# Kernel tuning notes

Measured on AMD Instinct MI355X. Metric: run time of the kernel, lower is better.

The kernel has to match this reference:

```python
import jax, jax.numpy as jnp
import numpy as np

N, E, D, L, NE, FF, G, V, H = 4096, 131072, 256, 4, 2, 512, 128, 100, 8
DK = D // H


def setup_inputs() -> dict:
    key = jax.random.key(0)
    ks = iter(jax.random.split(key, 64))
    def W(shape, scale=0.05):
        return jax.random.normal(next(ks), shape, dtype=jnp.float32) * scale
    inp = {}
    inp['z'] = jax.random.randint(next(ks), (N,), 0, V)
    inp['pos'] = jax.random.normal(next(ks), (N, 3), dtype=jnp.float32)
    inp['batch'] = jnp.sort(jax.random.randint(next(ks), (N,), 0, G))
    inp['edge_index'] = jax.random.randint(next(ks), (2, E), 0, N)
    inp['emb'] = W((V, D))
    # E_GCL stacks (EGNN layer: edge MLP, attention gate, node MLP)
    inp['egcl_edge_w1'] = W((L, 2 * D + 1, D)); inp['egcl_edge_b1'] = jnp.zeros((L, D), jnp.float32)
    inp['egcl_edge_w2'] = W((L, D, D));         inp['egcl_edge_b2'] = jnp.zeros((L, D), jnp.float32)
    inp['egcl_node_w1'] = W((L, 2 * D, D));     inp['egcl_node_b1'] = jnp.zeros((L, D), jnp.float32)
    inp['egcl_node_w2'] = W((L, D, D));         inp['egcl_node_b2'] = jnp.zeros((L, D), jnp.float32)
    inp['egcl_att_w'] = W((L, D, 1));           inp['egcl_att_b'] = jnp.zeros((L, 1), jnp.float32)
    # Transformer encoder stacks (post-norm)
    inp['enc_wq'] = W((NE, D, D)); inp['enc_bq'] = jnp.zeros((NE, D), jnp.float32)
    inp['enc_wk'] = W((NE, D, D)); inp['enc_bk'] = jnp.zeros((NE, D), jnp.float32)
    inp['enc_wv'] = W((NE, D, D)); inp['enc_bv'] = jnp.zeros((NE, D), jnp.float32)
    inp['enc_wo'] = W((NE, D, D)); inp['enc_bo'] = jnp.zeros((NE, D), jnp.float32)
    inp['enc_ln1_g'] = jnp.ones((NE, D), jnp.float32); inp['enc_ln1_b'] = jnp.zeros((NE, D), jnp.float32)
    inp['enc_ffn_w1'] = W((NE, D, FF)); inp['enc_ffn_b1'] = jnp.zeros((NE, FF), jnp.float32)
    inp['enc_ffn_w2'] = W((NE, FF, D)); inp['enc_ffn_b2'] = jnp.zeros((NE, D), jnp.float32)
    inp['enc_ln2_g'] = jnp.ones((NE, D), jnp.float32); inp['enc_ln2_b'] = jnp.zeros((NE, D), jnp.float32)
    # energy_fc head
    inp['fc_w1'] = W((D, D)); inp['fc_b1'] = jnp.zeros((D,), jnp.float32)
    inp['fc_w2'] = W((D, 1)); inp['fc_b2'] = jnp.zeros((1,), jnp.float32)
    return inp


def _layer_norm(x, g, b, eps=1e-5):
    mu = jnp.mean(x, axis=-1, keepdims=True)
    var = jnp.mean((x - mu) ** 2, axis=-1, keepdims=True)
    return (x - mu) * jax.lax.rsqrt(var + eps) * g + b


def reference(z, pos, batch, edge_index, emb,
              egcl_edge_w1, egcl_edge_b1, egcl_edge_w2, egcl_edge_b2,
              egcl_node_w1, egcl_node_b1, egcl_node_w2, egcl_node_b2,
              egcl_att_w, egcl_att_b,
              enc_wq, enc_bq, enc_wk, enc_bk, enc_wv, enc_bv, enc_wo, enc_bo,
              enc_ln1_g, enc_ln1_b, enc_ffn_w1, enc_ffn_b1, enc_ffn_w2, enc_ffn_b2,
              enc_ln2_g, enc_ln2_b, fc_w1, fc_b1, fc_w2, fc_b2):
    h = emb[z]                                   # [N, D]
    row, col = edge_index[0], edge_index[1]
    diff = pos[row] - pos[col]                   # static_coord: coords never updated
    radial = jnp.sum(diff * diff, axis=-1, keepdims=True)  # [E, 1]
    for i in range(L):
        m_in = jnp.concatenate([h[row], h[col], radial], axis=-1)     # [E, 2D+1]
        m = jax.nn.silu(m_in @ egcl_edge_w1[i] + egcl_edge_b1[i])
        m = jax.nn.silu(m @ egcl_edge_w2[i] + egcl_edge_b2[i])        # [E, D]
        m = m * jax.nn.sigmoid(m @ egcl_att_w[i] + egcl_att_b[i])     # attention gate
        agg = jax.ops.segment_sum(m, row, num_segments=N)             # [N, D]
        n_in = jnp.concatenate([h, agg], axis=-1)
        upd = jax.nn.silu(n_in @ egcl_node_w1[i] + egcl_node_b1[i]) @ egcl_node_w2[i] + egcl_node_b2[i]
        h = h + upd                                                   # residual
    scale = 1.0 / jnp.sqrt(jnp.asarray(DK, h.dtype))
    for i in range(NE):
        q = (h @ enc_wq[i] + enc_bq[i]).reshape(N, H, DK)
        k = (h @ enc_wk[i] + enc_bk[i]).reshape(N, H, DK)
        v = (h @ enc_wv[i] + enc_bv[i]).reshape(N, H, DK)
        scores = jnp.einsum('nhd,mhd->hnm', q, k) * scale
        a = jax.nn.softmax(scores, axis=-1)
        attn = jnp.einsum('hnm,mhd->nhd', a, v).reshape(N, D) @ enc_wo[i] + enc_bo[i]
        h = _layer_norm(h + attn, enc_ln1_g[i], enc_ln1_b[i])
        f = jax.nn.silu(h @ enc_ffn_w1[i] + enc_ffn_b1[i]) @ enc_ffn_w2[i] + enc_ffn_b2[i]
        h = _layer_norm(h + f, enc_ln2_g[i], enc_ln2_b[i])
    g = jax.ops.segment_sum(h, batch, num_segments=G)                 # scatter-add readout
    out = jax.nn.silu(g @ fc_w1 + fc_b1) @ fc_w2 + fc_b2              # [G, 1]
    return out
```

## Files before the change

### kernel.cpp

```cpp
#include <hip/hip_runtime.h>
#include <math.h>

#define N_NODES 4096
#define N_EDGES 131072
#define DIM     256
#define NL      4
#define NENC    2
#define FFD     512
#define NG      128
#define NHEAD   8
#define DKH     32
#define TE2     32

typedef __attribute__((ext_vector_type(8))) short bf16x8;
typedef __attribute__((ext_vector_type(4))) float f32x4;

__device__ __forceinline__ float siluf(float x) { return x / (1.f + __expf(-x)); }
__device__ __forceinline__ float sigmf_(float x) { return 1.f / (1.f + __expf(-x)); }
__device__ __forceinline__ unsigned short f2b(float f) {
    union { float f; unsigned u; } x; x.f = f;
    unsigned r = x.u + 0x7fffu + ((x.u >> 16) & 1u);
    return (unsigned short)(r >> 16);
}
__device__ __forceinline__ float b2f(unsigned short h) {
    union { unsigned u; float f; } x; x.u = (unsigned)h << 16; return x.f;
}

__global__ __launch_bounds__(256) void k_embed(const int* __restrict__ z,
                                               const float* __restrict__ emb,
                                               float* __restrict__ h) {
    int i = blockIdx.x * 256 + threadIdx.x;
    int n = i >> 8, d = i & 255;
    h[i] = emb[z[n] * DIM + d];
}

__global__ __launch_bounds__(256) void k_radial(const float* __restrict__ pos,
                                                const int* __restrict__ ei,
                                                float* __restrict__ radial) {
    int e = blockIdx.x * 256 + threadIdx.x;
    if (e >= N_EDGES) return;
    int r = ei[e], c = ei[N_EDGES + e];
    float dx = pos[r*3+0] - pos[c*3+0];
    float dy = pos[r*3+1] - pos[c*3+1];
    float dz = pos[r*3+2] - pos[c*3+2];
    radial[e] = dx*dx + dy*dy + dz*dz;
}

__global__ __launch_bounds__(256) void k_hist(const int* __restrict__ ei, int* __restrict__ cnt) {
    int e = blockIdx.x * 256 + threadIdx.x;
    if (e < N_EDGES) atomicAdd(&cnt[ei[e]], 1);
}

__global__ __launch_bounds__(256) void k_scan(const int* __restrict__ cnt, int* __restrict__ pos) {
    __shared__ int s_w[4];
    int t = threadIdx.x, lane = t & 63, wv = t >> 6;
    int loc[16]; int s = 0;
    #pragma unroll
    for (int i = 0; i < 16; ++i) { loc[i] = s; s += cnt[t * 16 + i]; }
    int inc = s;
    #pragma unroll
    for (int off = 1; off < 64; off <<= 1) {
        int v = __shfl_up(inc, off, 64);
        if (lane >= off) inc += v;
    }
    if (lane == 63) s_w[wv] = inc;
    __syncthreads();
    int wbase = 0;
    for (int j = 0; j < wv; ++j) wbase += s_w[j];
    int base = wbase + inc - s;
    #pragma unroll
    for (int i = 0; i < 16; ++i) pos[t * 16 + i] = base + loc[i];
}

__global__ __launch_bounds__(256) void k_scatter(const int* __restrict__ ei,
                                                 const float* __restrict__ radial,
                                                 int* __restrict__ pos,
                                                 int* __restrict__ rows_s,
                                                 int* __restrict__ cols_s,
                                                 float* __restrict__ rad_s) {
    int e = blockIdx.x * 256 + threadIdx.x;
    if (e >= N_EDGES) return;
    int r = ei[e];
    int p = atomicAdd(&pos[r], 1);
    rows_s[p] = r;
    cols_s[p] = ei[N_EDGES + e];
    rad_s[p] = radial[e];
}

__global__ __launch_bounds__(256) void k_conv_w2(const float* __restrict__ ew2,
                                                 unsigned short* __restrict__ W2F) {
    int tid = blockIdx.x * 256 + threadIdx.x;
    int layer = tid >> 13;
    int r = tid & 8191;
    int ks = r >> 10, ntg = (r >> 6) & 15, lane = r & 63;
    const float* W = ew2 + (size_t)layer * 65536;
    unsigned short tmp[8];
    #pragma unroll
    for (int j = 0; j < 8; ++j) {
        int k = ks*32 + 4*(lane>>4) + (j&3) + 16*(j>>2);
        int n = ntg*16 + (lane&15);
        tmp[j] = f2b(W[k*256 + n]);
    }
    *(bf16x8*)&W2F[(size_t)layer*65536 + (size_t)r*8] = *(const bf16x8*)&tmp[0];
}

__global__ __launch_bounds__(256) void k_pack_all(
    const float* __restrict__ ew1, const float* __restrict__ nw1, const float* __restrict__ nw2,
    const float* __restrict__ wq, const float* __restrict__ wk, const float* __restrict__ wv,
    const float* __restrict__ wo, const float* __restrict__ fw1, const float* __restrict__ fw2,
    unsigned short* __restrict__ dst)
{
    int f = blockIdx.x * 256 + threadIdx.x;
    int rem, panel, NTG, mode;
    if (f < 65536)       { rem = f;          panel = rem / 16384; rem &= 16383; NTG = 32; mode = 0; }
    else if (f < 131072) { rem = f - 65536;  panel = rem / 16384; rem &= 16383; NTG = 16; mode = 1; }
    else if (f < 163840) { rem = f - 131072; panel = rem / 8192;  rem &= 8191;  NTG = 16; mode = 2; }
    else if (f < 212992) { rem = f - 163840; panel = rem / 24576; rem %= 24576; NTG = 48; mode = 3; }
    else if (f < 229376) { rem = f - 212992; panel = rem / 8192;  rem &= 8191;  NTG = 16; mode = 4; }
    else if (f < 262144) { rem = f - 229376; panel = rem / 16384; rem &= 16383; NTG = 32; mode = 5; }
    else                 { rem = f - 262144; panel = rem / 16384; rem &= 16383; NTG = 16; mode = 6; }
    int ks   = rem / (NTG * 64);
    int ntg  = (rem >> 6) % NTG;
    int lane = rem & 63;
    unsigned short tmp[8];
    #pragma unroll
    for (int j = 0; j < 8; ++j) {
        int k = ks*32 + 4*(lane>>4) + (j&3) + 16*(j>>2);
        int n = ntg*16 + (lane&15);
        float val;
        switch (mode) {
            case 0: val = ew1[(size_t)panel*131328 + (n < 256 ? k*256 + n : (256 + k)*256 + (n - 256))]; break;
            case 1: val = nw1[(size_t)panel*131072 + k*256 + n]; break;
            case 2: val = nw2[(size_t)panel*65536 + k*256 + n]; break;
            case 3: { const float* b = (n < 256) ? wq : ((n < 512) ? wk : wv);
                      val = b[(size_t)panel*65536 + k*256 + (n & 255)]; } break;
            case 4: val = wo[(size_t)panel*65536 + k*256 + n]; break;
            case 5: val = fw1[(size_t)panel*131072 + k*512 + n]; break;
            default: val = fw2[(size_t)panel*131072 + k*256 + n]; break;
        }
        tmp[j] = f2b(val);
    }
    *(bf16x8*)&dst[(size_t)f * 8] = *(const bf16x8*)&tmp[0];
}

template<int NCHUNK, int NC, int NSPLIT, int ACT, int RESID, int OUTMODE>
__global__ __launch_bounds__(256) void k_gemm(
    const float* __restrict__ A0, const float* __restrict__ A1, int lda,
    const unsigned short* __restrict__ Wp,
    const float* __restrict__ b0, const float* __restrict__ b1, const float* __restrict__ b2,
    const float* __restrict__ resid, float* __restrict__ C,
    unsigned short* __restrict__ kpk, unsigned short* __restrict__ vpk)
{
    constexpr int NT  = NC / (64 * NSPLIT);
    constexpr int NTG = NC / 16;
    __shared__ __align__(16) char s_hi[16 * 512];
    __shared__ __align__(16) char s_lo[16 * 512];
    const int t = threadIdx.x, l = t & 63, w = t >> 6;
    const int g = l >> 4, r = l & 15;
    const int mtile  = blockIdx.x % 256;
    const int nchunk = blockIdx.x / 256;
    const int r0 = mtile * 16;

    f32x4 acc[NT];
    #pragma unroll
    for (int nt = 0; nt < NT; ++nt) acc[nt] = (f32x4){0.f, 0.f, 0.f, 0.f};

    const bf16x8* Wf = (const bf16x8*)Wp;
    for (int c = 0; c < NCHUNK; ++c) {
        const float* Ac = (c == 0) ? A0 : A1;
        __syncthreads();
        const int c4 = l * 4;
        #pragma unroll
        for (int it = 0; it < 4; ++it) {
            int row = it * 4 + w;
            float4 v = *(const float4*)&Ac[(size_t)(r0 + row) * lda + c4];
            float vv[4] = {v.x, v.y, v.z, v.w};
            ushort4 h4, l4;
            unsigned short hh;
            hh = f2b(vv[0]); h4.x = hh; l4.x = f2b(vv[0] - b2f(hh));
            hh = f2b(vv[1]); h4.y = hh; l4.y = f2b(vv[1] - b2f(hh));
            hh = f2b(vv[2]); h4.z = hh; l4.z = f2b(vv[2] - b2f(hh));
            hh = f2b(vv[3]); h4.w = hh; l4.w = f2b(vv[3] - b2f(hh));
            int boff = (c4 * 2) ^ (row << 3);
            *(ushort4*)&s_hi[row * 512 + boff] = h4;
            *(ushort4*)&s_lo[row * 512 + boff] = l4;
        }
        __syncthreads();
        #pragma unroll
        for (int ks = 0; ks < 8; ++ks) {
            const int ksg = c * 8 + ks;
            const int x0 = (ks * 64 + 8 * g) ^ (r << 3);
            union { uint2 u[2]; bf16x8 v; } ah, al;
            ah.u[0] = *(const uint2*)&s_hi[r * 512 + x0];
            ah.u[1] = *(const uint2*)&s_hi[r * 512 + (x0 ^ 32)];
            al.u[0] = *(const uint2*)&s_lo[r * 512 + x0];
            al.u[1] = *(const uint2*)&s_lo[r * 512 + (x0 ^ 32)];
            #pragma unroll
            for (int nt = 0; nt < NT; ++nt) {
                int fb = (nchunk * 4 + w) * NT + nt;
                bf16x8 bf_ = Wf[(size_t)(ksg * NTG + fb) * 64 + l];
                acc[nt] = __builtin_amdgcn_mfma_f32_16x16x32_bf16(ah.v, bf_, acc[nt], 0, 0, 0);
                acc[nt] = __builtin_amdgcn_mfma_f32_16x16x32_bf16(al.v, bf_, acc[nt], 0, 0, 0);
            }
        }
    }
    #pragma unroll
    for (int nt = 0; nt < NT; ++nt) {
        int n = ((nchunk * 4 + w) * NT + nt) * 16 + r;
        float bias = 0.f;
        if (b0) {
            const float* bp = (n < 256) ? b0 : ((n < 512) ? b1 : b2);
            bias = bp[n & 255];
        }
        #pragma unroll
        for (int reg = 0; reg < 4; ++reg) {
            int row = r0 + g * 4 + reg;
            float v = acc[nt][reg] + bias;
            if (ACT == 1) v = siluf(v);
            if (RESID) v += resid[(size_t)row * 256 + n];
            if (OUTMODE == 0) {
                C[(size_t)row * NC + n] = v;
            } else {
                if (n < 256) {
                    C[(size_t)row * 256 + n] = v;
                } else if (n < 512) {
                    int hd = (n - 256) >> 5, dm = (n - 256) & 31;
                    int dp = (dm & 3) | (((dm >> 4) & 1) << 2) | (((dm >> 2) & 3) << 3);
                    unsigned short hb = f2b(v);
                    size_t base = ((size_t)hd * N_NODES + row) * 64;
                    kpk[base + dp]      = hb;
                    kpk[base + 32 + dp] = f2b(v - b2f(hb));
                } else {
                    int hd = (n - 512) >> 5, dm = (n - 512) & 31;
                    int s = row & 31;
                    int sp = (s & 3) | (((s >> 4) & 1) << 2) | (((s >> 2) & 3) << 3);
                    int keyp = (row & ~31) | sp;
                    vpk[((size_t)hd * 32 + dm) * N_NODES + keyp] = f2b(v);
                }
            }
        }
    }
}

__global__ __launch_bounds__(256) void k_edge_mfma(
    const float* __restrict__ P12,
    const int* __restrict__ rows_s, const int* __restrict__ cols_s,
    const float* __restrict__ rad_s,
    const float* __restrict__ w1r, const float* __restrict__ b1,
    const unsigned short* __restrict__ W2F, const float* __restrict__ b2,
    const float* __restrict__ aw, const float* __restrict__ ab,
    float* __restrict__ agg)
{
    __shared__ __align__(16) char s_a[TE2 * 512];
    __shared__ int   s_row[TE2], s_cn[TE2];
    __shared__ float s_rad[TE2], s_gp[4][TE2], s_gate[TE2];
    const int t = threadIdx.x, l = t & 63, w = t >> 6;
    const int e0 = blockIdx.x * TE2;

    if (t < TE2) {
        s_row[t] = rows_s[e0 + t];
        s_cn[t]  = cols_s[e0 + t];
        s_rad[t] = rad_s[e0 + t];
    }
    __syncthreads();

    const int c4 = l * 4;
    const float4 wr = *(const float4*)&w1r[c4];
    const float4 bb = *(const float4*)&b1[c4];
    #pragma unroll
    for (int it = 0; it < 8; ++it) {
        int e = it * 4 + w;
        float4 pa = *(const float4*)&P12[(size_t)s_row[e] * 512 + c4];
        float4 pb = *(const float4*)&P12[(size_t)s_cn[e] * 512 + 256 + c4];
        float rad = s_rad[e];
        ushort4 pk;
        pk.x = f2b(siluf(pa.x + pb.x + rad * wr.x + bb.x));
        pk.y = f2b(siluf(pa.y + pb.y + rad * wr.y + bb.y));
        pk.z = f2b(siluf(pa.z + pb.z + rad * wr.z + bb.z));
        pk.w = f2b(siluf(pa.w + pb.w + rad * wr.w + bb.w));
        *(ushort4*)&s_a[e * 512 + ((c4 * 2) ^ ((e & 15) << 3))] = pk;
    }
    __syncthreads();

    const int g = l >> 4, r = l & 15;
    f32x4 acc[2][4];
    #pragma unroll
    for (int mt = 0; mt < 2; ++mt)
        #pragma unroll
        for (int nt = 0; nt < 4; ++nt)
            acc[mt][nt] = (f32x4){0.f, 0.f, 0.f, 0.f};

    const bf16x8* Wf = (const bf16x8*)W2F;
    for (int ks = 0; ks < 8; ++ks) {
        bf16x8 af[2], bfr[4];
        #pragma unroll
        for (int mt = 0; mt < 2; ++mt) {
            int rowa = mt * 16 + r;
            int x0 = (ks * 64 + 8 * g) ^ (r << 3);
            uint2 lo = *(const uint2*)&s_a[rowa * 512 + x0];
            uint2 hi = *(const uint2*)&s_a[rowa * 512 + (x0 ^ 32)];
            union { uint2 u[2]; bf16x8 v; } ua;
            ua.u[0] = lo; ua.u[1] = hi;
            af[mt] = ua.v;
        }
        #pragma unroll
        for (int nt = 0; nt < 4; ++nt)
            bfr[nt] = Wf[(ks * 16 + w * 4 + nt) * 64 + l];
        #pragma unroll
        for (int mt = 0; mt < 2; ++mt)
            #pragma unroll
            for (int nt = 0; nt < 4; ++nt)
                acc[mt][nt] = __builtin_amdgcn_mfma_f32_16x16x32_bf16(af[mt], bfr[nt], acc[mt][nt], 0, 0, 0);
    }

    float b2v[4], awv[4];
    #pragma unroll
    for (int nt = 0; nt < 4; ++nt) {
        int col = w * 64 + nt * 16 + r;
        b2v[nt] = b2[col];
        awv[nt] = aw[col];
    }
    float pg[2][4];
    #pragma unroll
    for (int mt = 0; mt < 2; ++mt)
        #pragma unroll
        for (int reg = 0; reg < 4; ++reg) {
            float s = 0.f;
            #pragma unroll
            for (int nt = 0; nt < 4; ++nt) {
                float v = siluf(acc[mt][nt][reg] + b2v[nt]);
                acc[mt][nt][reg] = v;
                s += v * awv[nt];
            }
            pg[mt][reg] = s;
        }
    #pragma unroll
    for (int off = 1; off < 16; off <<= 1)
        #pragma unroll
        for (int mt = 0; mt < 2; ++mt)
            #pragma unroll
            for (int reg = 0; reg < 4; ++reg)
                pg[mt][reg] += __shfl_xor(pg[mt][reg], off, 64);
    if (r == 0) {
        #pragma unroll
        for (int mt = 0; mt < 2; ++mt)
            #pragma unroll
            for (int reg = 0; reg < 4; ++reg)
                s_gp[w][mt * 16 + g * 4 + reg] = pg[mt][reg];
    }
    __syncthreads();
    if (t < TE2)
        s_gate[t] = sigmf_(s_gp[0][t] + s_gp[1][t] + s_gp[2][t] + s_gp[3][t] + ab[0]);
    __syncthreads();

    unsigned short* s_out = (unsigned short*)s_a;
    #pragma unroll
    for (int mt = 0; mt < 2; ++mt)
        #pragma unroll
        for (int reg = 0; reg < 4; ++reg) {
            int el = mt * 16 + g * 4 + reg;
            float gt = s_gate[el];
            #pragma unroll
            for (int nt = 0; nt < 4; ++nt)
                s_out[el * 256 + w * 64 + nt * 16 + r] = f2b(acc[mt][nt][reg] * gt);
        }
    __syncthreads();
    float cur = 0.f;
    for (int e = 0; e < TE2; ++e) {
        cur += b2f(s_out[e * 256 + t]);
        bool flush = (e == TE2 - 1) || (s_row[e + 1] != s_row[e]);
        if (flush) {
            atomicAdd(&agg[(size_t)s_row[e] * DIM + t], cur);
            cur = 0.f;
        }
    }
}

template<int ACT>
__global__ __launch_bounds__(256) void k_mlp_small(
    const float* __restrict__ A1, const float* __restrict__ W,
    const float* __restrict__ bias, float* __restrict__ C)
{
    __shared__ float s_a[16][260];
    const int t  = threadIdx.x;
    const int r0 = blockIdx.x * 16;
    for (int r = 0; r < 16; ++r)
        s_a[r][t] = A1[(size_t)(r0 + r) * DIM + t];
    __syncthreads();
    const int er0 = (t >> 6) * 4;
    const int c0 = (t & 63) * 4;
    float acc[4][4];
    #pragma unroll
    for (int e = 0; e < 4; ++e)
        #pragma unroll
        for (int c = 0; c < 4; ++c) acc[e][c] = 0.f;
    #pragma unroll 2
    for (int k = 0; k < DIM; k += 4) {
        float4 w0 = *(const float4*)&W[(size_t)(k+0)*DIM + c0];
        float4 w1 = *(const float4*)&W[(size_t)(k+1)*DIM + c0];
        float4 w2 = *(const float4*)&W[(size_t)(k+2)*DIM + c0];
        float4 w3 = *(const float4*)&W[(size_t)(k+3)*DIM + c0];
        #pragma unroll
        for (int e = 0; e < 4; ++e) {
            float4 x = *(const float4*)&s_a[er0+e][k];
            acc[e][0] += x.x*w0.x + x.y*w1.x + x.z*w2.x + x.w*w3.x;
            acc[e][1] += x.x*w0.y + x.y*w1.y + x.z*w2.y + x.w*w3.y;
            acc[e][2] += x.x*w0.z + x.y*w1.z + x.z*w2.z + x.w*w3.z;
            acc[e][3] += x.x*w0.w + x.y*w1.w + x.z*w2.w + x.w*w3.w;
        }
    }
    float4 bb = *(const float4*)&bias[c0];
    #pragma unroll
    for (int e = 0; e < 4; ++e) {
        float v0 = acc[e][0] + bb.x, v1 = acc[e][1] + bb.y;
        float v2 = acc[e][2] + bb.z, v3 = acc[e][3] + bb.w;
        if (ACT == 1) { v0 = siluf(v0); v1 = siluf(v1); v2 = siluf(v2); v3 = siluf(v3); }
        float4 o; o.x = v0; o.y = v1; o.z = v2; o.w = v3;
        *(float4*)&C[(size_t)(r0 + er0 + e) * DIM + c0] = o;
    }
}

__global__ __launch_bounds__(256) void k_ln(const float* __restrict__ x,
                                            const float* __restrict__ g,
                                            const float* __restrict__ b,
                                            float* __restrict__ out) {
    int t = threadIdx.x, lane = t & 63, w = t >> 6;
    int row = blockIdx.x * 4 + w;
    float4 v = *(const float4*)&x[(size_t)row * DIM + lane * 4];
    float s = v.x + v.y + v.z + v.w;
    #pragma unroll
    for (int off = 32; off; off >>= 1) s += __shfl_xor(s, off, 64);
    float mu = s * (1.f / 256.f);
    float dx = v.x - mu, dy = v.y - mu, dz = v.z - mu, dw = v.w - mu;
    float q = dx*dx + dy*dy + dz*dz + dw*dw;
    #pragma unroll
    for (int off = 32; off; off >>= 1) q += __shfl_xor(q, off, 64);
    float rs = rsqrtf(q * (1.f / 256.f) + 1e-5f);
    float4 gg = *(const float4*)&g[lane * 4];
    float4 bb = *(const float4*)&b[lane * 4];
    float4 o;
    o.x = dx * rs * gg.x + bb.x;
    o.y = dy * rs * gg.y + bb.y;
    o.z = dz * rs * gg.z + bb.z;
    o.w = dw * rs * gg.w + bb.w;
    *(float4*)&out[(size_t)row * DIM + lane * 4] = o;
}

__global__ __launch_bounds__(256) void k_attn_mfma(
    const float* __restrict__ q,
    const unsigned short* __restrict__ kpk,
    const unsigned short* __restrict__ vpk,
    float* __restrict__ o)
{
    __shared__ __align__(16) char s_k[2][8192];
    __shared__ __align__(16) char s_v[2][4096];
    const int t = threadIdx.x, lane = t & 63, w = t >> 6;
    const int g = lane >> 4, r = lane & 15;
    const int head = blockIdx.y;
    const int q0 = blockIdx.x * 64;
    const float scale = 0.17677669529663687f;

    bf16x8 qh, ql;
    {
        const float* qp = &q[(size_t)(q0 + w*16 + r) * DIM + head*DKH + 4*g];
        float4 f0 = *(const float4*)qp;
        float4 f1 = *(const float4*)(qp + 16);
        float vv[8] = {f0.x, f0.y, f0.z, f0.w, f1.x, f1.y, f1.z, f1.w};
        union { unsigned short s[8]; bf16x8 v; } uh, ul;
        #pragma unroll
        for (int j = 0; j < 8; ++j) {
            float sv = vv[j] * scale;
            unsigned short hb = f2b(sv);
            uh.s[j] = hb;
            ul.s[j] = f2b(sv - b2f(hb));
        }
        qh = uh.v; ql = ul.v;
    }

    const char* kbase = (const char*)(kpk + (size_t)head * N_NODES * 64);
    const unsigned short* vbase = vpk + (size_t)head * 32 * N_NODES;
    const int vrow = t >> 3, vch = t & 7;

    uint4 kr0, kr1, vr0;
    {
        const char* kt = kbase;
        kr0 = *(const uint4*)(kt + t * 16);
        kr1 = *(const uint4*)(kt + 4096 + t * 16);
        vr0 = *(const uint4*)(vbase + (size_t)vrow * N_NODES + vch * 8);
        int key0 = t >> 3, sl0 = t & 7;
        *(uint4*)&s_k[0][key0 * 128 + ((sl0 ^ (key0 & 7)) << 4)] = kr0;
        int c1 = t + 256, key1 = c1 >> 3, sl1 = c1 & 7;
        *(uint4*)&s_k[0][key1 * 128 + ((sl1 ^ (key1 & 7)) << 4)] = kr1;
        *(uint4*)&s_v[0][vrow * 128 + ((vch ^ (vrow & 7)) << 4)] = vr0;
    }
    __syncthreads();

    float m = -1e30f, l = 0.f;
    f32x4 ot0 = (f32x4){0.f,0.f,0.f,0.f}, ot1 = (f32x4){0.f,0.f,0.f,0.f};

    for (int tile = 0; tile < 64; ++tile) {
        const int cur = tile & 1;
        if (tile < 63) {
            const char* kt = kbase + (size_t)(tile + 1) * 8192;
            kr0 = *(const uint4*)(kt + t * 16);
            kr1 = *(const uint4*)(kt + 4096 + t * 16);
            vr0 = *(const uint4*)(vbase + (size_t)vrow * N_NODES + (tile + 1) * 64 + vch * 8);
        }
        bf16x8 kh[4], kl[4];
        #pragma unroll
        for (int kb = 0; kb < 4; ++kb) {
            int key = kb * 16 + r;
            kh[kb] = *(const bf16x8*)&s_k[cur][key * 128 + ((g ^ (r & 7)) << 4)];
            kl[kb] = *(const bf16x8*)&s_k[cur][key * 128 + (((4 + g) ^ (r & 7)) << 4)];
        }
        f32x4 sc[4];
        #pragma unroll
        for (int kb = 0; kb < 4; ++kb) {
            f32x4 a = (f32x4){0.f,0.f,0.f,0.f};
            a = __builtin_amdgcn_mfma_f32_16x16x32_bf16(kh[kb], qh, a, 0, 0, 0);
            a = __builtin_amdgcn_mfma_f32_16x16x32_bf16(kh[kb], ql, a, 0, 0, 0);
            a = __builtin_amdgcn_mfma_f32_16x16x32_bf16(kl[kb], qh, a, 0, 0, 0);
            sc[kb] = a;
        }
        float tm = -1e30f;
        #pragma unroll
        for (int kb = 0; kb < 4; ++kb)
            #pragma unroll
            for (int e = 0; e < 4; ++e) tm = fmaxf(tm, sc[kb][e]);
        tm = fmaxf(tm, __shfl_xor(tm, 16, 64));
        tm = fmaxf(tm, __shfl_xor(tm, 32, 64));
        float nm = fmaxf(m, tm);
        float scf = __expf(m - nm);
        m = nm;
        float p[16]; float ls = 0.f;
        #pragma unroll
        for (int kb = 0; kb < 4; ++kb)
            #pragma unroll
            for (int e = 0; e < 4; ++e) {
                float pe = __expf(sc[kb][e] - nm);
                p[kb*4+e] = pe; ls += pe;
            }
        ls += __shfl_xor(ls, 16, 64);
        ls += __shfl_xor(ls, 32, 64);
        l = l * scf + ls;
        ot0[0] *= scf; ot0[1] *= scf; ot0[2] *= scf; ot0[3] *= scf;
        ot1[0] *= scf; ot1[1] *= scf; ot1[2] *= scf; ot1[3] *= scf;
        union { unsigned short s[8]; bf16x8 v; } pk0, pk1;
        #pragma unroll
        for (int j = 0; j < 8; ++j) {
            pk0.s[j] = f2b(p[(j >> 2) * 4 + (j & 3)]);
            pk1.s[j] = f2b(p[(2 + (j >> 2)) * 4 + (j & 3)]);
        }
        bf16x8 vf00 = *(const bf16x8*)&s_v[cur][(0*16 + r) * 128 + (((0*4 + g) ^ (r & 7)) << 4)];
        bf16x8 vf01 = *(const bf16x8*)&s_v[cur][(0*16 + r) * 128 + (((1*4 + g) ^ (r & 7)) << 4)];
        bf16x8 vf10 = *(const bf16x8*)&s_v[cur][(1*16 + r) * 128 + (((0*4 + g) ^ (r & 7)) << 4)];
        bf16x8 vf11 = *(const bf16x8*)&s_v[cur][(1*16 + r) * 128 + (((1*4 + g) ^ (r & 7)) << 4)];
        ot0 = __builtin_amdgcn_mfma_f32_16x16x32_bf16(vf00, pk0.v, ot0, 0, 0, 0);
        ot0 = __builtin_amdgcn_mfma_f32_16x16x32_bf16(vf01, pk1.v, ot0, 0, 0, 0);
        ot1 = __builtin_amdgcn_mfma_f32_16x16x32_bf16(vf10, pk0.v, ot1, 0, 0, 0);
        ot1 = __builtin_amdgcn_mfma_f32_16x16x32_bf16(vf11, pk1.v, ot1, 0, 0, 0);

        __syncthreads();
        if (tile < 63) {
            int key0 = t >> 3, sl0 = t & 7;
            *(uint4*)&s_k[cur ^ 1][key0 * 128 + ((sl0 ^ (key0 & 7)) << 4)] = kr0;
            int c1 = t + 256, key1 = c1 >> 3, sl1 = c1 & 7;
            *(uint4*)&s_k[cur ^ 1][key1 * 128 + ((sl1 ^ (key1 & 7)) << 4)] = kr1;
            *(uint4*)&s_v[cur ^ 1][vrow * 128 + ((vch ^ (vrow & 7)) << 4)] = vr0;
        }
        __syncthreads();
    }

    float inv = 1.f / l;
    float* op = &o[(size_t)(q0 + w*16 + r) * DIM + head*DKH];
    *(float4*)(op + 4*g)      = make_float4(ot0[0]*inv, ot0[1]*inv, ot0[2]*inv, ot0[3]*inv);
    *(float4*)(op + 16 + 4*g) = make_float4(ot1[0]*inv, ot1[1]*inv, ot1[2]*inv, ot1[3]*inv);
}

__global__ __launch_bounds__(256) void k_segsum(const float* __restrict__ h,
                                                const int* __restrict__ batch,
                                                float* __restrict__ gbuf) {
    int i = blockIdx.x * 256 + threadIdx.x;
    int n = i >> 8, d = i & 255;
    atomicAdd(&gbuf[batch[n] * DIM + d], h[i]);
}

__global__ __launch_bounds__(256) void k_head2(const float* __restrict__ gmid,
                                               const float* __restrict__ w2,
                                               const float* __restrict__ b2,
                                               float* __restrict__ out) {
    int t = threadIdx.x, lane = t & 63, w = t >> 6;
    int g = blockIdx.x * 4 + w;
    float4 x  = *(const float4*)&gmid[g * DIM + lane * 4];
    float4 ww = *(const float4*)&w2[lane * 4];
    float s = x.x * ww.x + x.y * ww.y + x.z * ww.z + x.w * ww.w;
    #pragma unroll
    for (int off = 32; off; off >>= 1) s += __shfl_xor(s, off, 64);
    if (lane == 0) out[g] = s + b2[0];
}

extern "C" void kernel_launch(void* const* d_in, const int* in_sizes, int n_in,
                              void* d_out, int out_size, void* d_ws, size_t ws_size,
                              hipStream_t stream)
{
    const int*   z     = (const int*)d_in[0];
    const float* pos   = (const float*)d_in[1];
    const int*   batch = (const int*)d_in[2];
    const int*   ei    = (const int*)d_in[3];
    const float* emb   = (const float*)d_in[4];
    const float* ew1   = (const float*)d_in[5];
    const float* eb1   = (const float*)d_in[6];
    const float* ew2   = (const float*)d_in[7];
    const float* eb2   = (const float*)d_in[8];
    const float* nw1   = (const float*)d_in[9];
    const float* nb1   = (const float*)d_in[10];
    const float* nw2   = (const float*)d_in[11];
    const float* nb2   = (const float*)d_in[12];
    const float* aw    = (const float*)d_in[13];
    const float* ab    = (const float*)d_in[14];
    const float* wq    = (const float*)d_in[15];
    const float* bq    = (const float*)d_in[16];
    const float* wk    = (const float*)d_in[17];
    const float* bk    = (const float*)d_in[18];
    const float* wv    = (const float*)d_in[19];
    const float* bv    = (const float*)d_in[20];
    const float* wo    = (const float*)d_in[21];
    const float* bo    = (const float*)d_in[22];
    const float* ln1g  = (const float*)d_in[23];
    const float* ln1b  = (const float*)d_in[24];
    const float* fw1   = (const float*)d_in[25];
    const float* fb1   = (const float*)d_in[26];
    const float* fw2   = (const float*)d_in[27];
    const float* fb2   = (const float*)d_in[28];
    const float* ln2g  = (const float*)d_in[29];
    const float* ln2b  = (const float*)d_in[30];
    const float* fcw1  = (const float*)d_in[31];
    const float* fcb1  = (const float*)d_in[32];
    const float* fcw2  = (const float*)d_in[33];
    const float* fcb2  = (const float*)d_in[34];
    float* out = (float*)d_out;

    float* ws = (float*)d_ws;
    const size_t ND = (size_t)N_NODES * DIM;
    float* h    = ws;
    float* agg  = ws + ND;
    float* A    = ws + 2 * ND;
    float* U    = ws + 3 * ND;
    float* Bffn = ws + 6 * ND;
    unsigned short* kpk = (unsigned short*)Bffn;
    unsigned short* vpk = kpk + (size_t)NHEAD * N_NODES * 64;
    float* radial = Bffn + (3 * ND) / 2;
    int*   cnt    = (int*)(radial + N_EDGES);
    int*   pcur   = cnt + N_NODES;
    float* gbuf   = ws + 8 * ND;
    float* gmid   = gbuf + (size_t)NG * DIM;
    float* rad_s  = gmid + (size_t)NG * DIM;
    int*   rows_s = (int*)(rad_s + N_EDGES);
    int*   cols_s = rows_s + N_EDGES;
    unsigned short* W2F   = (unsigned short*)(cols_s + N_EDGES);
    unsigned short* packs = W2F + (size_t)NL * 65536;

    unsigned short* PK_W1   = packs;
    unsigned short* PK_NW1  = packs + 524288;
    unsigned short* PK_NW2  = packs + 1048576;
    unsigned short* PK_QKV  = packs + 1310720;
    unsigned short* PK_WO   = packs + 1703936;
    unsigned short* PK_FFN1 = packs + 1835008;
    unsigned short* PK_FFN2 = packs + 2097152;

    dim3 b256(256);

    k_embed<<<N_NODES * DIM / 256, b256, 0, stream>>>(z, emb, h);
    k_radial<<<N_EDGES / 256, b256, 0, stream>>>(pos, ei, radial);
    k_conv_w2<<<NL * 8192 / 256, b256, 0, stream>>>(ew2, W2F);
    k_pack_all<<<1152, b256, 0, stream>>>(ew1, nw1, nw2, wq, wk, wv, wo, fw1, fw2, packs);

    hipMemsetAsync(cnt, 0, N_NODES * sizeof(int), stream);
    k_hist<<<N_EDGES / 256, b256, 0, stream>>>(ei, cnt);
    k_scan<<<1, b256, 0, stream>>>(cnt, pcur);
    k_scatter<<<N_EDGES / 256, b256, 0, stream>>>(ei, radial, pcur, rows_s, cols_s, rad_s);

    for (int l = 0; l < NL; ++l) {
        hipMemsetAsync(agg, 0, ND * sizeof(float), stream);
        const float* W1l = ew1 + (size_t)l * 513 * DIM;
        k_gemm<1,512,2,0,0,0><<<512, b256, 0, stream>>>(h, nullptr, DIM,
            PK_W1 + (size_t)l * 131072, nullptr, nullptr, nullptr, nullptr, U,
            nullptr, nullptr);
        k_edge_mfma<<<N_EDGES / TE2, b256, 0, stream>>>(U, rows_s, cols_s, rad_s,
            W1l + (size_t)512 * DIM, eb1 + (size_t)l * DIM,
            W2F + (size_t)l * 65536, eb2 + (size_t)l * DIM,
            aw + (size_t)l * DIM, ab + l, agg);
        const float* nb1l = nb1 + (size_t)l * DIM;
        k_gemm<2,256,2,1,0,0><<<512, b256, 0, stream>>>(h, agg, DIM,
            PK_NW1 + (size_t)l * 131072, nb1l, nb1l, nb1l, nullptr, A,
            nullptr, nullptr);
        const float* nb2l = nb2 + (size_t)l * DIM;
        k_gemm<1,256,2,0,1,0><<<512, b256, 0, stream>>>(A, nullptr, DIM,
            PK_NW2 + (size_t)l * 65536, nb2l, nb2l, nb2l, h, h,
            nullptr, nullptr);
    }

    for (int i = 0; i < NENC; ++i) {
        k_gemm<1,768,3,0,0,1><<<768, b256, 0, stream>>>(h, nullptr, DIM,
            PK_QKV + (size_t)i * 196608,
            bq + (size_t)i * DIM, bk + (size_t)i * DIM, bv + (size_t)i * DIM, nullptr, U,
            kpk, vpk);
        dim3 ag(N_NODES / 64, NHEAD);
        k_attn_mfma<<<ag, b256, 0, stream>>>(U, kpk, vpk, A);
        const float* bol = bo + (size_t)i * DIM;
        k_gemm<1,256,2,0,1,0><<<512, b256, 0, stream>>>(A, nullptr, DIM,
            PK_WO + (size_t)i * 65536, bol, bol, bol, h, agg,
            nullptr, nullptr);
        k_ln<<<N_NODES / 4, b256, 0, stream>>>(agg, ln1g + (size_t)i * DIM, ln1b + (size_t)i * DIM, h);
        const float* fb1l = fb1 + (size_t)i * FFD;
        k_gemm<1,512,2,1,0,0><<<512, b256, 0, stream>>>(h, nullptr, DIM,
            PK_FFN1 + (size_t)i * 131072, fb1l, fb1l + 256, nullptr, nullptr, Bffn,
            nullptr, nullptr);
        const float* fb2l = fb2 + (size_t)i * DIM;
        k_gemm<2,256,2,0,1,0><<<512, b256, 0, stream>>>(Bffn, Bffn + 256, FFD,
            PK_FFN2 + (size_t)i * 131072, fb2l, fb2l, fb2l, h, agg,
            nullptr, nullptr);
        k_ln<<<N_NODES / 4, b256, 0, stream>>>(agg, ln2g + (size_t)i * DIM, ln2b + (size_t)i * DIM, h);
    }

    hipMemsetAsync(gbuf, 0, (size_t)NG * DIM * sizeof(float), stream);
    k_segsum<<<N_NODES * DIM / 256, b256, 0, stream>>>(h, batch, gbuf);
    k_mlp_small<1><<<NG / 16, b256, 0, stream>>>(gbuf, fcw1, fcb1, gmid);
    k_head2<<<NG / 4, b256, 0, stream>>>(gmid, fcw2, fcb2, out);
}
```

Baseline: 676.3 us.

## Split attention over two key halves with merge kernel; transpose edge output staging

The attention kernel now splits the key range into two halves across a third grid dimension. Each split writes unnormalized partial outputs plus its running max and sum, and a new merge kernel combines them with a log-sum-exp rescale. This doubles the number of attention blocks from 512 to 1024 to fill more compute units, at the cost of an extra kernel launch and an extra read and write of partial buffers. Separately, the edge kernel stages gated outputs transposed (column-major, padded stride 40) using ushort4 stores and uint4 reads, which cuts LDS transactions in the segment reduction.

```diff
diff --git a/kernel.cpp b/kernel.cpp
--- a/kernel.cpp
+++ b/kernel.cpp
@@ -251,7 +251,7 @@
     const float* __restrict__ aw, const float* __restrict__ ab,
     float* __restrict__ agg)
 {
-    __shared__ __align__(16) char s_a[TE2 * 512];
+    __shared__ __align__(16) char s_a[20480];
     __shared__ int   s_row[TE2], s_cn[TE2];
     __shared__ float s_rad[TE2], s_gp[4][TE2], s_gate[TE2];
     const int t = threadIdx.x, l = t & 63, w = t >> 6;
@@ -355,23 +355,34 @@
 
     unsigned short* s_out = (unsigned short*)s_a;
     #pragma unroll
-    for (int mt = 0; mt < 2; ++mt)
-        #pragma unroll
-        for (int reg = 0; reg < 4; ++reg) {
-            int el = mt * 16 + g * 4 + reg;
-            float gt = s_gate[el];
-            #pragma unroll
-            for (int nt = 0; nt < 4; ++nt)
-                s_out[el * 256 + w * 64 + nt * 16 + r] = f2b(acc[mt][nt][reg] * gt);
-        }
+    for (int mt = 0; mt < 2; ++mt) {
+        float4 gt4 = *(const float4*)&s_gate[mt * 16 + g * 4];
+        #pragma unroll
+        for (int nt = 0; nt < 4; ++nt) {
+            int col = w * 64 + nt * 16 + r;
+            ushort4 o4;
+            o4.x = f2b(acc[mt][nt][0] * gt4.x);
+            o4.y = f2b(acc[mt][nt][1] * gt4.y);
+            o4.z = f2b(acc[mt][nt][2] * gt4.z);
+            o4.w = f2b(acc[mt][nt][3] * gt4.w);
+            *(ushort4*)&s_out[col * 40 + mt * 16 + g * 4] = o4;
+        }
+    }
     __syncthreads();
     float cur = 0.f;
-    for (int e = 0; e < TE2; ++e) {
-        cur += b2f(s_out[e * 256 + t]);
-        bool flush = (e == TE2 - 1) || (s_row[e + 1] != s_row[e]);
-        if (flush) {
-            atomicAdd(&agg[(size_t)s_row[e] * DIM + t], cur);
-            cur = 0.f;
+    #pragma unroll
+    for (int c = 0; c < 4; ++c) {
+        union { uint4 q; unsigned short s[8]; } ch;
+        ch.q = *(const uint4*)&s_out[t * 40 + c * 8];
+        #pragma unroll
+        for (int j = 0; j < 8; ++j) {
+            int e = c * 8 + j;
+            cur += b2f(ch.s[j]);
+            bool flush = (e == TE2 - 1) || (s_row[e + 1] != s_row[e]);
+            if (flush) {
+                atomicAdd(&agg[(size_t)s_row[e] * DIM + t], cur);
+                cur = 0.f;
+            }
         }
     }
 }
@@ -450,13 +461,15 @@
     const float* __restrict__ q,
     const unsigned short* __restrict__ kpk,
     const unsigned short* __restrict__ vpk,
-    float* __restrict__ o)
+    float* __restrict__ opart0, float* __restrict__ opart1,
+    float* __restrict__ mlbuf)
 {
     __shared__ __align__(16) char s_k[2][8192];
     __shared__ __align__(16) char s_v[2][4096];
     const int t = threadIdx.x, lane = t & 63, w = t >> 6;
     const int g = lane >> 4, r = lane & 15;
     const int head = blockIdx.y;
+    const int split = blockIdx.z;
     const int q0 = blockIdx.x * 64;
     const float scale = 0.17677669529663687f;
 
@@ -477,8 +490,9 @@
         qh = uh.v; ql = ul.v;
     }
 
-    const char* kbase = (const char*)(kpk + (size_t)head * N_NODES * 64);
+    const char* kbase = (const char*)(kpk + (size_t)head * N_NODES * 64) + (size_t)split * 32 * 8192;
     const unsigned short* vbase = vpk + (size_t)head * 32 * N_NODES;
+    const int koff = split * 2048;
     const int vrow = t >> 3, vch = t & 7;
 
     uint4 kr0, kr1, vr0;
@@ -486,7 +500,7 @@
         const char* kt = kbase;
         kr0 = *(const uint4*)(kt + t * 16);
         kr1 = *(const uint4*)(kt + 4096 + t * 16);
-        vr0 = *(const uint4*)(vbase + (size_t)vrow * N_NODES + vch * 8);
+        vr0 = *(const uint4*)(vbase + (size_t)vrow * N_NODES + koff + vch * 8);
         int key0 = t >> 3, sl0 = t & 7;
         *(uint4*)&s_k[0][key0 * 128 + ((sl0 ^ (key0 & 7)) << 4)] = kr0;
         int c1 = t + 256, key1 = c1 >> 3, sl1 = c1 & 7;
@@ -498,13 +512,13 @@
     float m = -1e30f, l = 0.f;
     f32x4 ot0 = (f32x4){0.f,0.f,0.f,0.f}, ot1 = (f32x4){0.f,0.f,0.f,0.f};
 
-    for (int tile = 0; tile < 64; ++tile) {
+    for (int tile = 0; tile < 32; ++tile) {
         const int cur = tile & 1;
-        if (tile < 63) {
+        if (tile < 31) {
             const char* kt = kbase + (size_t)(tile + 1) * 8192;
             kr0 = *(const uint4*)(kt + t * 16);
             kr1 = *(const uint4*)(kt + 4096 + t * 16);
-            vr0 = *(const uint4*)(vbase + (size_t)vrow * N_NODES + (tile + 1) * 64 + vch * 8);
+            vr0 = *(const uint4*)(vbase + (size_t)vrow * N_NODES + koff + (tile + 1) * 64 + vch * 8);
         }
         bf16x8 kh[4], kl[4];
         #pragma unroll
@@ -561,7 +575,7 @@
         ot1 = __builtin_amdgcn_mfma_f32_16x16x32_bf16(vf11, pk1.v, ot1, 0, 0, 0);
 
         __syncthreads();
-        if (tile < 63) {
+        if (tile < 31) {
             int key0 = t >> 3, sl0 = t & 7;
             *(uint4*)&s_k[cur ^ 1][key0 * 128 + ((sl0 ^ (key0 & 7)) << 4)] = kr0;
             int c1 = t + 256, key1 = c1 >> 3, sl1 = c1 & 7;
@@ -571,10 +585,28 @@
         __syncthreads();
     }
 
-    float inv = 1.f / l;
-    float* op = &o[(size_t)(q0 + w*16 + r) * DIM + head*DKH];
-    *(float4*)(op + 4*g)      = make_float4(ot0[0]*inv, ot0[1]*inv, ot0[2]*inv, ot0[3]*inv);
-    *(float4*)(op + 16 + 4*g) = make_float4(ot1[0]*inv, ot1[1]*inv, ot1[2]*inv, ot1[3]*inv);
+    float* op = (split == 0 ? opart0 : opart1) + (size_t)(q0 + w*16 + r) * DIM + head*DKH;
+    *(float4*)(op + 4*g)      = make_float4(ot0[0], ot0[1], ot0[2], ot0[3]);
+    *(float4*)(op + 16 + 4*g) = make_float4(ot1[0], ot1[1], ot1[2], ot1[3]);
+    if (g == 0) {
+        float* mp = &mlbuf[(((size_t)split * NHEAD + head) * N_NODES + q0 + w*16 + r) * 2];
+        mp[0] = m; mp[1] = l;
+    }
+}
+
+__global__ __launch_bounds__(256) void k_attn_merge(
+    const float* __restrict__ o0, const float* __restrict__ o1,
+    const float* __restrict__ ml, float* __restrict__ A)
+{
+    int i = blockIdx.x * 256 + threadIdx.x;
+    int qq = i >> 8, head = (i & 255) >> 5;
+    const float* p0 = &ml[((size_t)head * N_NODES + qq) * 2];
+    const float* p1 = &ml[(((size_t)NHEAD + head) * N_NODES + qq) * 2];
+    float m0 = p0[0], l0 = p0[1], m1 = p1[0], l1 = p1[1];
+    float mm = fmaxf(m0, m1);
+    float e0 = __expf(m0 - mm), e1 = __expf(m1 - mm);
+    float inv = 1.f / (e0 * l0 + e1 * l1);
+    A[i] = (o0[i] * e0 + o1[i] * e1) * inv;
 }
 
 __global__ __launch_bounds__(256) void k_segsum(const float* __restrict__ h,
@@ -646,6 +678,8 @@
     float* agg  = ws + ND;
     float* A    = ws + 2 * ND;
     float* U    = ws + 3 * ND;
+    float* op0  = ws + 4 * ND;
+    float* op1  = ws + 5 * ND;
     float* Bffn = ws + 6 * ND;
     unsigned short* kpk = (unsigned short*)Bffn;
     unsigned short* vpk = kpk + (size_t)NHEAD * N_NODES * 64;
@@ -705,8 +739,9 @@
             PK_QKV + (size_t)i * 196608,
             bq + (size_t)i * DIM, bk + (size_t)i * DIM, bv + (size_t)i * DIM, nullptr, U,
             kpk, vpk);
-        dim3 ag(N_NODES / 64, NHEAD);
-        k_attn_mfma<<<ag, b256, 0, stream>>>(U, kpk, vpk, A);
+        dim3 ag(N_NODES / 64, NHEAD, 2);
+        k_attn_mfma<<<ag, b256, 0, stream>>>(U, kpk, vpk, op0, op1, agg);
+        k_attn_merge<<<N_NODES * DIM / 256, b256, 0, stream>>>(op0, op1, agg, A);
         const float* bol = bo + (size_t)i * DIM;
         k_gemm<1,256,2,0,1,0><<<512, b256, 0, stream>>>(A, nullptr, DIM,
             PK_WO + (size_t)i * 65536, bol, bol, bol, h, agg,
```

Result: no change. 670.0 us (-0.9%).
